# Kernel tuning notes

Measured on AMD Instinct MI355X. Metric: run time of the kernel, lower is better.

## Reference

```python
import jax, jax.numpy as jnp
import numpy as np

B, T = 4, 2048
D_MODEL = 1024
N_HEADS = 8
HEAD_DIM = 256
KV_LRANK = 64


def _orthogonalize_per_head(w):
    """Muon Split: per-head Newton-Schulz 2-step orthogonalization.
    w: [n_heads*head_dim, d_model]; head_dim (256) <= d_model (1024), so the
    rows<=cols branch of the torch code always applies."""
    chunks = w.reshape(N_HEADS, HEAD_DIM, D_MODEL)
    def ns(m):
        A = m @ m.T                                  # [hd, hd]
        Bm = 1.5 * jnp.eye(HEAD_DIM, dtype=m.dtype) - 0.5 * A
        return Bm @ m
    return jax.vmap(ns)(chunks).reshape(w.shape)


def setup_inputs() -> dict:
    key = jax.random.key(0)
    ks = jax.random.split(key, 6)
    def lin(k, out_dim, in_dim):
        # kaiming-uniform-ish scale like nn.Linear default
        bound = 1.0 / np.sqrt(in_dim)
        return jax.random.uniform(k, (out_dim, in_dim), jnp.float32, -bound, bound)
    Wq = _orthogonalize_per_head(lin(ks[0], N_HEADS * HEAD_DIM, D_MODEL))
    return {
        "x": jax.random.normal(ks[1], (B, T, D_MODEL), jnp.float32),
        "Wq": Wq,
        "Wkv_down": lin(ks[2], KV_LRANK, D_MODEL),
        "Wk_up": lin(ks[3], N_HEADS * HEAD_DIM, KV_LRANK),
        "Wv_up": lin(ks[4], N_HEADS * HEAD_DIM, KV_LRANK),
        "Wo": lin(ks[5], D_MODEL, N_HEADS * HEAD_DIM),
    }


def reference(x, Wq, Wkv_down, Wk_up, Wv_up, Wo):
    b, t, _ = x.shape
    q = (x @ Wq.T).reshape(b, t, N_HEADS, HEAD_DIM)          # [B,T,H,hd]
    kv_latent = x @ Wkv_down.T                               # [B,T,r]
    k = (kv_latent @ Wk_up.T).reshape(b, t, N_HEADS, HEAD_DIM)
    v = (kv_latent @ Wv_up.T).reshape(b, t, N_HEADS, HEAD_DIM)
    scale = HEAD_DIM ** (-0.5)
    scores = jnp.einsum('bqhd,bkhd->bhqk', q, k) * scale     # [B,H,T,T]
    attn = jax.nn.softmax(scores, axis=-1)
    out = jnp.einsum('bhqk,bkhd->bqhd', attn, v)             # [B,T,H,hd]
    out = out.reshape(b, t, N_HEADS * HEAD_DIM)
    return out @ Wo.T                                        # [B,T,d_model]
```

## Files before the change

kernel.cpp:

```cpp
#include <hip/hip_runtime.h>
#include <hip/hip_bf16.h>
#include <math.h>

typedef __bf16 bf16_t;
typedef bf16_t bf16x8 __attribute__((ext_vector_type(8)));
typedef bf16_t bf16x4 __attribute__((ext_vector_type(4)));
typedef float f32x4 __attribute__((ext_vector_type(4)));
typedef float f32x16 __attribute__((ext_vector_type(16)));

#define DEV_INLINE __device__ __forceinline__

constexpr int B_ = 4, T_ = 2048, DM = 1024, NH = 8, RK = 64;
constexpr int BT = B_ * T_;
constexpr int QC = NH * RK;
constexpr int CQW = RK + QC;
#define QK_SCALE 0.09016844f

__global__ void cast_f32_bf16(const float* __restrict__ in, bf16_t* __restrict__ out, int n) {
  int i = (blockIdx.x * blockDim.x + threadIdx.x) * 4;
  if (i >= n) return;
  const float4 v = *reinterpret_cast<const float4*>(in + i);
  bf16x4 o;
  o[0] = (bf16_t)v.x; o[1] = (bf16_t)v.y; o[2] = (bf16_t)v.z; o[3] = (bf16_t)v.w;
  *reinterpret_cast<bf16x4*>(out + i) = o;
}

__global__ void build_wq_eff(const float* __restrict__ Wku, const float* __restrict__ Wq,
                             bf16_t* __restrict__ out) {
  const int m = blockIdx.x * 256 + threadIdx.x;
  const int h = blockIdx.y;
  const int r0 = blockIdx.z * 4;
  float s[4] = {};
  const float* wk = Wku + (size_t)h * 256 * 64 + r0;
  const float* wq = Wq + (size_t)h * 256 * 1024 + m;
  for (int d = 0; d < 256; ++d) {
    float qv = wq[(size_t)d * 1024];
#pragma unroll
    for (int j = 0; j < 4; ++j) s[j] += wk[d * 64 + j] * qv;
  }
#pragma unroll
  for (int j = 0; j < 4; ++j)
    out[(size_t)(h * 64 + r0 + j) * 1024 + m] = (bf16_t)(s[j] * QK_SCALE);
}

__global__ void build_w_eff(const float* __restrict__ Wo, const float* __restrict__ Wvu,
                            bf16_t* __restrict__ out) {
  const int m0 = blockIdx.x * 4;
  const int h = blockIdx.y * 4 + (threadIdx.x >> 6);
  const int r = threadIdx.x & 63;
  float s[4] = {};
  const float* wv = Wvu + (size_t)h * 256 * 64 + r;
  const float* wo = Wo + (size_t)m0 * 2048 + h * 256;
  for (int d = 0; d < 256; ++d) {
    const float wvv = wv[d * 64];
#pragma unroll
    for (int j = 0; j < 4; ++j) s[j] += wo[(size_t)j * 2048 + d] * wvv;
  }
#pragma unroll
  for (int j = 0; j < 4; ++j)
    out[(size_t)(m0 + j) * 512 + h * 64 + r] = (bf16_t)s[j];
}

__global__ void transpose_c(const bf16_t* __restrict__ cq, bf16_t* __restrict__ cT) {
  __shared__ bf16_t tile[64][65];
  const int b = blockIdx.y;
  const int t0 = blockIdx.x * 64;
  const int tx = threadIdx.x & 63;
  const int ty = threadIdx.x >> 6;
#pragma unroll
  for (int i = 0; i < 16; ++i) {
    int t = ty * 16 + i;
    tile[t][tx] = cq[((size_t)b * T_ + t0 + t) * CQW + tx];
  }
  __syncthreads();
#pragma unroll
  for (int i = 0; i < 16; ++i) {
    int r = ty * 16 + i;
    cT[((size_t)b * RK + r) * T_ + t0 + tx] = tile[tx][r];
  }
}

DEV_INLINE void storeC(float* p, float v) { *p = v; }
DEV_INLINE void storeC(bf16_t* p, float v) { *p = (bf16_t)v; }

DEV_INLINE void async_load16(const void* g, void* l) {
  __builtin_amdgcn_global_load_lds((__attribute__((address_space(1))) void*)g,
                                   (__attribute__((address_space(3))) void*)l, 16, 0, 0);
}

template <typename OutT>
__global__ __launch_bounds__(256) void gemm_bt(const bf16_t* __restrict__ A,
                                               const bf16_t* __restrict__ Bm,
                                               OutT* __restrict__ C, int M, int N, int K) {
  __shared__ bf16_t lA[128 * 32];
  __shared__ bf16_t lB[128 * 32];
  const int tid = threadIdx.x;
  const int lane = tid & 63;
  const int w = tid >> 6;
  const int lo = lane & 15, hi = lane >> 4;
  const int wr = w >> 1, wc = w & 1;
  const size_t row0 = (size_t)blockIdx.x * 128;
  const size_t col0 = (size_t)blockIdx.y * 128;
  const int w64 = w * 64;
  f32x4 acc[4][4] = {};

  for (int k0 = 0; k0 < K; k0 += 32) {
    __syncthreads();
#pragma unroll
    for (int j = 0; j < 2; ++j) {
      const int chunk = j * 256 + w64 + lane;
      const int r = chunk >> 2;
      const int kk = (chunk & 3) * 8;
      const bf16_t* gA = A + (row0 + r) * K + (k0 + kk);
      async_load16(gA, &lA[(size_t)(j * 256 + w64) * 8]);
      size_t rB = col0 + r;
      if (rB >= (size_t)N) rB = N - 1;
      const bf16_t* gB = Bm + rB * K + (k0 + kk);
      async_load16(gB, &lB[(size_t)(j * 256 + w64) * 8]);
    }
    __syncthreads();
    const bf16x8* pA = reinterpret_cast<const bf16x8*>(lA);
    const bf16x8* pB = reinterpret_cast<const bf16x8*>(lB);
    bf16x8 af[4], bfr[4];
#pragma unroll
    for (int m = 0; m < 4; ++m) af[m] = pA[(wr * 64 + m * 16 + lo) * 4 + hi];
#pragma unroll
    for (int n = 0; n < 4; ++n) bfr[n] = pB[(wc * 64 + n * 16 + lo) * 4 + hi];
#pragma unroll
    for (int m = 0; m < 4; ++m)
#pragma unroll
      for (int n = 0; n < 4; ++n)
        acc[m][n] = __builtin_amdgcn_mfma_f32_16x16x32_bf16(af[m], bfr[n], acc[m][n], 0, 0, 0);
  }
#pragma unroll
  for (int m = 0; m < 4; ++m)
#pragma unroll
    for (int n = 0; n < 4; ++n)
#pragma unroll
      for (int q = 0; q < 4; ++q) {
        const size_t row = row0 + wr * 64 + m * 16 + hi * 4 + q;
        const size_t col = col0 + wc * 64 + n * 16 + lo;
        if ((int)col < N) storeC(&C[row * N + col], acc[m][n][q]);
      }
}

__global__ __launch_bounds__(256) void attn_kernel(const bf16_t* __restrict__ CQ,
                                                   const bf16_t* __restrict__ CT,
                                                   bf16_t* __restrict__ U) {
  constexpr int KVT = 64;
  constexpr int NT = T_ / KVT;
  constexpr int BUFE = KVT * 64;
  __shared__ bf16_t Kl[2][KVT][64];
  __shared__ bf16_t Vl[2][64][KVT];
  const int tid = threadIdx.x;
  const int w = tid >> 6, lane = tid & 63;
  const int lq = lane & 31;
  const int hi = lane >> 5;
  const int b = blockIdx.z;
  const int h = blockIdx.y;
  const size_t qrow = (size_t)b * T_ + blockIdx.x * 128 + w * 32;
  const bf16_t* __restrict__ cq = CQ + (size_t)b * T_ * CQW;
  const bf16_t* __restrict__ ct = CT + (size_t)b * RK * T_;

  const int srow = w * 8 + (lane >> 3);
  const int schunk = (lane & 7) ^ (lane >> 3);

  bf16x8 qf[4];
#pragma unroll
  for (int kc = 0; kc < 4; ++kc)
    qf[kc] = *reinterpret_cast<const bf16x8*>(
        CQ + (qrow + lq) * CQW + RK + h * RK + kc * 16 + hi * 8);

  f32x16 acc0 = {}, acc1 = {}, accl = {};

  bf16x8 onesf;
#pragma unroll
  for (int j = 0; j < 8; ++j) onesf[j] = (bf16_t)1.0f;

  const bf16_t* const kl = &Kl[0][0][0];
  const bf16_t* const vl = &Vl[0][0][0];
  const int xr = lq & 7;
  int kch[4], vch[2][2];
#pragma unroll
  for (int kc = 0; kc < 4; ++kc) kch[kc] = ((((kc << 1) | hi)) ^ xr) * 8;
#pragma unroll
  for (int sub = 0; sub < 2; ++sub)
#pragma unroll
    for (int kc = 0; kc < 2; ++kc)
      vch[sub][kc] = ((((sub << 2) | (kc << 1) | hi)) ^ xr) * 8;
  const int roff0 = lq * 64, roff1 = (32 + lq) * 64;

#pragma unroll
  for (int q = 0; q < 2; ++q) {
    async_load16(cq + (size_t)(q * 32 + srow) * CQW + schunk * 8,
                 &Kl[0][q * 32 + w * 8][0]);
    async_load16(ct + (size_t)(q * 32 + srow) * T_ + schunk * 8,
                 &Vl[0][q * 32 + w * 8][0]);
  }

  for (int t = 0; t < NT; ++t) {
    const int cur = t & 1;
    const int cbo = cur * BUFE;
    if (t + 1 < NT) {
      const int kvn = (t + 1) * KVT;
#pragma unroll
      for (int q = 0; q < 2; ++q) {
        async_load16(cq + (size_t)(kvn + q * 32 + srow) * CQW + schunk * 8,
                     &Kl[cur ^ 1][q * 32 + w * 8][0]);
        async_load16(ct + (size_t)(q * 32 + srow) * T_ + kvn + schunk * 8,
                     &Vl[cur ^ 1][q * 32 + w * 8][0]);
      }
      asm volatile("s_waitcnt vmcnt(4)" ::: "memory");
    } else {
      asm volatile("s_waitcnt vmcnt(0)" ::: "memory");
    }
    __builtin_amdgcn_s_barrier();
    __builtin_amdgcn_sched_barrier(0);

#pragma unroll
    for (int sub = 0; sub < 2; ++sub) {
      const int krb = cbo + (sub ? roff1 : roff0);
      bf16x8 kf[4];
#pragma unroll
      for (int kc = 0; kc < 4; ++kc)
        kf[kc] = *reinterpret_cast<const bf16x8*>(kl + krb + kch[kc]);
      f32x16 s = {};
#pragma unroll
      for (int kc = 0; kc < 4; ++kc)
        s = __builtin_amdgcn_mfma_f32_32x32x16_bf16(kf[kc], qf[kc], s, 0, 0, 0);

      float p[16];
#pragma unroll
      for (int i = 0; i < 16; ++i) p[i] = __builtin_amdgcn_exp2f(s[i]);

      unsigned pw[8];
#pragma unroll
      for (int i = 0; i < 8; ++i)
        asm("v_cvt_pk_bf16_f32 %0, %1, %2" : "=v"(pw[i]) : "v"(p[2 * i]), "v"(p[2 * i + 1]));
      asm("v_permlane32_swap_b32 %0, %1" : "+v"(pw[0]), "+v"(pw[2]));
      asm("v_permlane32_swap_b32 %0, %1" : "+v"(pw[1]), "+v"(pw[3]));
      asm("v_permlane32_swap_b32 %0, %1" : "+v"(pw[4]), "+v"(pw[6]));
      asm("v_permlane32_swap_b32 %0, %1" : "+v"(pw[5]), "+v"(pw[7]));
      union { unsigned u[4]; bf16x8 v; } pb0, pb1;
      pb0.u[0] = pw[0]; pb0.u[1] = pw[1]; pb0.u[2] = pw[2]; pb0.u[3] = pw[3];
      pb1.u[0] = pw[4]; pb1.u[1] = pw[5]; pb1.u[2] = pw[6]; pb1.u[3] = pw[7];

      bf16x8 vf0[2], vf1[2];
#pragma unroll
      for (int kc = 0; kc < 2; ++kc) {
        vf0[kc] = *reinterpret_cast<const bf16x8*>(vl + cbo + roff0 + vch[sub][kc]);
        vf1[kc] = *reinterpret_cast<const bf16x8*>(vl + cbo + roff1 + vch[sub][kc]);
      }

      acc0 = __builtin_amdgcn_mfma_f32_32x32x16_bf16(vf0[0], pb0.v, acc0, 0, 0, 0);
      acc0 = __builtin_amdgcn_mfma_f32_32x32x16_bf16(vf0[1], pb1.v, acc0, 0, 0, 0);
      acc1 = __builtin_amdgcn_mfma_f32_32x32x16_bf16(vf1[0], pb0.v, acc1, 0, 0, 0);
      acc1 = __builtin_amdgcn_mfma_f32_32x32x16_bf16(vf1[1], pb1.v, acc1, 0, 0, 0);
      accl = __builtin_amdgcn_mfma_f32_32x32x16_bf16(onesf, pb0.v, accl, 0, 0, 0);
      accl = __builtin_amdgcn_mfma_f32_32x32x16_bf16(onesf, pb1.v, accl, 0, 0, 0);
    }

    __builtin_amdgcn_sched_barrier(0);
    __builtin_amdgcn_s_barrier();
  }

  const float inv = 1.0f / accl[0];
  const size_t ubase = (qrow + lq) * QC + h * RK;
#pragma unroll
  for (int g = 0; g < 4; ++g) {
    bf16x4 o0, o1;
#pragma unroll
    for (int j = 0; j < 4; ++j) {
      o0[j] = (bf16_t)(acc0[g * 4 + j] * inv);
      o1[j] = (bf16_t)(acc1[g * 4 + j] * inv);
    }
    const int d0 = g * 8 + hi * 4;
    *reinterpret_cast<bf16x4*>(U + ubase + d0) = o0;
    *reinterpret_cast<bf16x4*>(U + ubase + 32 + d0) = o1;
  }
}

extern "C" void kernel_launch(void* const* d_in, const int* in_sizes, int n_in,
                              void* d_out, int out_size, void* d_ws, size_t ws_size,
                              hipStream_t stream) {
  const float* x   = (const float*)d_in[0];
  const float* Wq  = (const float*)d_in[1];
  const float* Wkd = (const float*)d_in[2];
  const float* Wku = (const float*)d_in[3];
  const float* Wvu = (const float*)d_in[4];
  const float* Wo  = (const float*)d_in[5];
  float* out = (float*)d_out;

  char* ws = (char*)d_ws;
  bf16_t* xb    = (bf16_t*)(ws + 0);
  bf16_t* CQb   = (bf16_t*)(ws + 16777216);
  bf16_t* Ub    = (bf16_t*)(ws + 26214400);
  bf16_t* Wcat  = (bf16_t*)(ws + 34603008);
  bf16_t* Wfe   = (bf16_t*)(ws + 35782656);
  bf16_t* cTb   = (bf16_t*)(ws + 36831232);

  cast_f32_bf16<<<8192, 256, 0, stream>>>(x, xb, BT * DM);
  cast_f32_bf16<<<64, 256, 0, stream>>>(Wkd, Wcat, RK * DM);
  build_wq_eff<<<dim3(4, 8, 16), 256, 0, stream>>>(Wku, Wq, Wcat + (size_t)RK * DM);
  build_w_eff<<<dim3(256, 2), 256, 0, stream>>>(Wo, Wvu, Wfe);

  gemm_bt<bf16_t><<<dim3(BT / 128, 5), 256, 0, stream>>>(xb, Wcat, CQb, BT, CQW, DM);
  transpose_c<<<dim3(T_ / 64, B_), 256, 0, stream>>>(CQb, cTb);
  attn_kernel<<<dim3(T_ / 128, NH, B_), 256, 0, stream>>>(CQb, cTb, Ub);
  gemm_bt<float><<<dim3(BT / 128, DM / 128), 256, 0, stream>>>(Ub, Wfe, out, BT, DM, QC);
}
```

Before: 148.1 us.

## Fuse latent transpose into projection GEMM epilogue and raise MFMA priority

The separate transpose_c kernel is removed. The first GEMM's epilogue now writes the transposed latent (columns 0-63, tiles with blockIdx.y==0 and wc==0) straight into cT as bf16x4 vectors, which saves one launch and one extra read of the latent. The attention kernel also wraps its MFMA groups in s_setprio(1)/s_setprio(0) so that waves issuing matrix ops get scheduling priority over waves doing exp and conversions. The trade-off is extra stores in the GEMM epilogue on a subset of tiles.

```diff
diff --git a/kernel.cpp b/kernel.cpp
--- a/kernel.cpp
+++ b/kernel.cpp
@@ -61,25 +61,6 @@
     out[(size_t)(m0 + j) * 512 + h * 64 + r] = (bf16_t)s[j];
 }
 
-__global__ void transpose_c(const bf16_t* __restrict__ cq, bf16_t* __restrict__ cT) {
-  __shared__ bf16_t tile[64][65];
-  const int b = blockIdx.y;
-  const int t0 = blockIdx.x * 64;
-  const int tx = threadIdx.x & 63;
-  const int ty = threadIdx.x >> 6;
-#pragma unroll
-  for (int i = 0; i < 16; ++i) {
-    int t = ty * 16 + i;
-    tile[t][tx] = cq[((size_t)b * T_ + t0 + t) * CQW + tx];
-  }
-  __syncthreads();
-#pragma unroll
-  for (int i = 0; i < 16; ++i) {
-    int r = ty * 16 + i;
-    cT[((size_t)b * RK + r) * T_ + t0 + tx] = tile[tx][r];
-  }
-}
-
 DEV_INLINE void storeC(float* p, float v) { *p = v; }
 DEV_INLINE void storeC(bf16_t* p, float v) { *p = (bf16_t)v; }
 
@@ -88,10 +69,12 @@
                                    (__attribute__((address_space(3))) void*)l, 16, 0, 0);
 }
 
-template <typename OutT>
+template <typename OutT, bool WRITE_CT>
 __global__ __launch_bounds__(256) void gemm_bt(const bf16_t* __restrict__ A,
                                                const bf16_t* __restrict__ Bm,
-                                               OutT* __restrict__ C, int M, int N, int K) {
+                                               OutT* __restrict__ C,
+                                               bf16_t* __restrict__ CT,
+                                               int M, int N, int K) {
   __shared__ bf16_t lA[128 * 32];
   __shared__ bf16_t lB[128 * 32];
   const int tid = threadIdx.x;
@@ -142,6 +125,21 @@
         const size_t col = col0 + wc * 64 + n * 16 + lo;
         if ((int)col < N) storeC(&C[row * N + col], acc[m][n][q]);
       }
+  if (WRITE_CT && blockIdx.y == 0 && wc == 0) {
+#pragma unroll
+    for (int m = 0; m < 4; ++m)
+#pragma unroll
+      for (int n = 0; n < 4; ++n) {
+        bf16x4 o;
+#pragma unroll
+        for (int q = 0; q < 4; ++q) o[q] = (bf16_t)acc[m][n][q];
+        const size_t row = row0 + wr * 64 + m * 16 + hi * 4;
+        const int bb = (int)(row >> 11);
+        const int t0 = (int)(row & (T_ - 1));
+        const int r = n * 16 + lo;
+        *reinterpret_cast<bf16x4*>(CT + ((size_t)bb * RK + r) * T_ + t0) = o;
+      }
+  }
 }
 
 __global__ __launch_bounds__(256) void attn_kernel(const bf16_t* __restrict__ CQ,
@@ -225,9 +223,11 @@
       for (int kc = 0; kc < 4; ++kc)
         kf[kc] = *reinterpret_cast<const bf16x8*>(kl + krb + kch[kc]);
       f32x16 s = {};
+      __builtin_amdgcn_s_setprio(1);
 #pragma unroll
       for (int kc = 0; kc < 4; ++kc)
         s = __builtin_amdgcn_mfma_f32_32x32x16_bf16(kf[kc], qf[kc], s, 0, 0, 0);
+      __builtin_amdgcn_s_setprio(0);
 
       float p[16];
 #pragma unroll
@@ -252,12 +252,14 @@
         vf1[kc] = *reinterpret_cast<const bf16x8*>(vl + cbo + roff1 + vch[sub][kc]);
       }
 
+      __builtin_amdgcn_s_setprio(1);
       acc0 = __builtin_amdgcn_mfma_f32_32x32x16_bf16(vf0[0], pb0.v, acc0, 0, 0, 0);
       acc0 = __builtin_amdgcn_mfma_f32_32x32x16_bf16(vf0[1], pb1.v, acc0, 0, 0, 0);
       acc1 = __builtin_amdgcn_mfma_f32_32x32x16_bf16(vf1[0], pb0.v, acc1, 0, 0, 0);
       acc1 = __builtin_amdgcn_mfma_f32_32x32x16_bf16(vf1[1], pb1.v, acc1, 0, 0, 0);
       accl = __builtin_amdgcn_mfma_f32_32x32x16_bf16(onesf, pb0.v, accl, 0, 0, 0);
       accl = __builtin_amdgcn_mfma_f32_32x32x16_bf16(onesf, pb1.v, accl, 0, 0, 0);
+      __builtin_amdgcn_s_setprio(0);
     }
 
     __builtin_amdgcn_sched_barrier(0);
@@ -304,8 +306,7 @@
   build_wq_eff<<<dim3(4, 8, 16), 256, 0, stream>>>(Wku, Wq, Wcat + (size_t)RK * DM);
   build_w_eff<<<dim3(256, 2), 256, 0, stream>>>(Wo, Wvu, Wfe);
 
-  gemm_bt<bf16_t><<<dim3(BT / 128, 5), 256, 0, stream>>>(xb, Wcat, CQb, BT, CQW, DM);
-  transpose_c<<<dim3(T_ / 64, B_), 256, 0, stream>>>(CQb, cTb);
+  gemm_bt<bf16_t, true><<<dim3(BT / 128, 5), 256, 0, stream>>>(xb, Wcat, CQb, cTb, BT, CQW, DM);
   attn_kernel<<<dim3(T_ / 128, NH, B_), 256, 0, stream>>>(CQb, cTb, Ub);
-  gemm_bt<float><<<dim3(BT / 128, DM / 128), 256, 0, stream>>>(Ub, Wfe, out, BT, DM, QC);
-}
+  gemm_bt<float, false><<<dim3(BT / 128, DM / 128), 256, 0, stream>>>(Ub, Wfe, out, nullptr, BT, DM, QC);
+}
```

After: 145.9 us. Within noise of the previous version (-1.5%).
